# Optimization experiments

Measured on AMD Instinct MI355X. Metric: run time of the kernel, lower is better.

The kernel has to match this reference:

```python
import jax, jax.numpy as jnp
import numpy as np

FEATURE_SIZE = 512
NUM_CLASSES = 64
HIDDEN = 256
BATCH = 256
SEQ_LEN = 512


def setup_inputs() -> dict:
    key = jax.random.key(0)
    ks = jax.random.split(key, 8)
    in_dim = FEATURE_SIZE + NUM_CLASSES
    s = 0.05
    return {
        "x": jax.random.normal(ks[0], (BATCH, SEQ_LEN, FEATURE_SIZE), dtype=jnp.float32),
        "tag": jax.random.randint(ks[1], (BATCH, SEQ_LEN), 0, NUM_CLASSES, dtype=jnp.int32),
        # LSTM params, torch gate order (i, f, g, o)
        "W_ih": jax.random.normal(ks[2], (4 * HIDDEN, in_dim), dtype=jnp.float32) * s,
        "W_hh": jax.random.normal(ks[3], (4 * HIDDEN, HIDDEN), dtype=jnp.float32) * s,
        "b_ih": jax.random.normal(ks[4], (4 * HIDDEN,), dtype=jnp.float32) * s,
        "b_hh": jax.random.normal(ks[5], (4 * HIDDEN,), dtype=jnp.float32) * s,
        # output projection
        "W_out": jax.random.normal(ks[6], (NUM_CLASSES, HIDDEN), dtype=jnp.float32) * s,
        "b_out": jax.random.normal(ks[7], (NUM_CLASSES,), dtype=jnp.float32) * s,
    }


def reference(x, tag, W_ih, W_hh, b_ih, b_hh, W_out, b_out):
    # x: [B, S, F], tag: [B, S] -> scalar summed CE loss (ignore_index=-1).
    # Dropout omitted (eval-mode identity) for a deterministic reference.
    B, S, F = x.shape
    C = W_out.shape[0]
    xs = jnp.transpose(x, (1, 0, 2))      # [S, B, F] time-major
    tags = jnp.transpose(tag, (1, 0))     # [S, B]

    h0 = jnp.zeros((B, HIDDEN), dtype=x.dtype)
    c0 = jnp.zeros((B, HIDDEN), dtype=x.dtype)
    p0 = jnp.zeros((B,), dtype=jnp.int32)  # initial prev_tag = 0

    def step(carry, inputs):
        h, c, pred = carry
        xi, ti = inputs                         # [B,F], [B]
        onehot = jax.nn.one_hot(pred, C, dtype=xi.dtype)
        inp = jnp.concatenate([xi, onehot], axis=1)          # [B, F+C]
        gates = inp @ W_ih.T + b_ih + h @ W_hh.T + b_hh      # [B, 4H]
        i_g, f_g, g_g, o_g = jnp.split(gates, 4, axis=1)
        i_g = jax.nn.sigmoid(i_g)
        f_g = jax.nn.sigmoid(f_g)
        g_g = jnp.tanh(g_g)
        o_g = jax.nn.sigmoid(o_g)
        c_new = f_g * c + i_g * g_g
        h_new = o_g * jnp.tanh(c_new)
        logits = h_new @ W_out.T + b_out                     # [B, C]
        pred_new = jnp.argmax(logits, axis=1).astype(jnp.int32)
        logp = jax.nn.log_softmax(logits, axis=1)
        valid = ti != -1
        ti_safe = jnp.where(valid, ti, 0)
        nll = -jnp.take_along_axis(logp, ti_safe[:, None], axis=1)[:, 0]
        loss = jnp.sum(jnp.where(valid, nll, 0.0))
        return (h_new, c_new, pred_new), loss

    _, losses = jax.lax.scan(step, (h0, c0, p0), (xs, tags))
    return jnp.sum(losses)
```

## Files before the change

kernel.cpp:

```cpp
#include <hip/hip_runtime.h>

typedef unsigned int u32;
typedef unsigned short u16;
typedef short bf16x8 __attribute__((ext_vector_type(8)));
typedef u16 u16x8 __attribute__((ext_vector_type(8)));
typedef float f32x4 __attribute__((ext_vector_type(4)));
typedef _Float16 h2v __attribute__((ext_vector_type(2)));

#define HID 256
#define NCLS 64
#define GATES 1024
#define SEQ 512
#define NBATCH 256
#define FEAT 512
#define INDIM 576

__device__ __forceinline__ u16 f2b(float f) {
  u32 u = __builtin_bit_cast(u32, f);
  u += 0x7fffu + ((u >> 16) & 1u);
  return (u16)(u >> 16);
}
__device__ __forceinline__ float b2f(u16 v) {
  u32 u = ((u32)v) << 16;
  return __builtin_bit_cast(float, u);
}
__device__ __forceinline__ u32 packh2(float a, float b) {
  u16 lo = __builtin_bit_cast(u16, (_Float16)a);
  u16 hi = __builtin_bit_cast(u16, (_Float16)b);
  return (u32)lo | ((u32)hi << 16);
}
__device__ __forceinline__ float fdot2a(u32 h, u32 w, float c) {
#if __has_builtin(__builtin_amdgcn_fdot2)
  return __builtin_amdgcn_fdot2(__builtin_bit_cast(h2v, h),
                                __builtin_bit_cast(h2v, w), c, false);
#else
  h2v a = __builtin_bit_cast(h2v, h);
  h2v b = __builtin_bit_cast(h2v, w);
  return c + (float)a[0] * (float)b[0] + (float)a[1] * (float)b[1];
#endif
}
__device__ __forceinline__ float sigmf_(float x) { return 1.f / (1.f + __expf(-x)); }
__device__ __forceinline__ float tanhf_(float x) { return 1.f - 2.f / (1.f + __expf(2.f * x)); }

__global__ void prep_kernel(const float* __restrict__ W_ih, const float* __restrict__ W_hh,
                            const float* __restrict__ W_out,
                            u16* __restrict__ Wihk, u32* __restrict__ WhhF,
                            u32* __restrict__ WhhL2, u32* __restrict__ WoutR,
                            float* __restrict__ Woh2, float* __restrict__ out) {
  int idx = blockIdx.x * 256 + threadIdx.x;
  const int N0 = 1024 * 512;
  const int N1 = N0 + 48 * 512 * 4;
  const int N2 = N1 + 16 * 512 * 4;
  const int N3 = N2 + 16 * 512;
  const int N4 = N3 + 64 * 256 * 4;
  if (idx < N0) {
    int g = idx >> 9, k = idx & 511;
    Wihk[idx] = f2b(W_ih[g * INDIM + k]);
  } else if (idx < N1) {
    int r = idx - N0;
    int q = r & 3, u4 = r >> 2;
    int t = u4 & 511, i = u4 >> 9;
    int j = i >> 3, qq = i & 7;
    int kqv = t >> 7, glv = t & 127;
    int g = glv + j * 128;
    int k = kqv * 64 + qq * 8 + 2 * q;
    WhhF[r] = packh2(W_hh[g * HID + k], W_hh[g * HID + k + 1]);
  } else if (idx < N2) {
    int r = idx - N1;
    int q = r & 3, u4 = r >> 2;
    int t = u4 & 511, i2 = u4 >> 9;
    int j = 6 + (i2 >> 3), qq = i2 & 7;
    int kqv = t >> 7, glv = t & 127;
    int g = glv + j * 128;
    int k = kqv * 64 + qq * 8 + 2 * q;
    WhhL2[r] = packh2(W_hh[g * HID + k], W_hh[g * HID + k + 1]);
  } else if (idx < N3) {
    int r = idx - N2;
    int j = r >> 9, t = r & 511;
    int cc = t & 63, kqv = t >> 6;
    int k0 = kqv * 32 + 2 * j;
    WoutR[r] = packh2(W_out[cc * HID + k0], W_out[cc * HID + k0 + 1]);
  } else if (idx < N4) {
    int r = idx - N3;
    int jj = r & 3, c = (r >> 2) & 255, p = r >> 10;
    Woh2[r] = W_ih[(jj * 256 + c) * INDIM + FEAT + p];
  } else if (idx == N4) {
    out[0] = 0.f;
  }
}

__global__ __launch_bounds__(256) void gemm_xp(const float* __restrict__ x,
                                               const u16* __restrict__ Wihk,
                                               const float* __restrict__ b_ih,
                                               const float* __restrict__ b_hh,
                                               u16* __restrict__ Xp) {
  __shared__ u16 As[128 * 32];
  __shared__ u16 Bs[128 * 32];
  const int tid = threadIdx.x;
  const int bx = blockIdx.x;
  const int m0 = (bx >> 3) * 128;
  const int n0 = (bx & 7) * 128;
  const int wave = tid >> 6, lane = tid & 63;
  const int wm = (wave >> 1) * 64, wn = (wave & 1) * 64;
  const int l16 = lane & 15, quad = lane >> 4;
  const int r = tid >> 2;
  const int c8 = (tid & 3) * 8;

  f32x4 zero4 = {0.f, 0.f, 0.f, 0.f};
  f32x4 acc[4][4];
#pragma unroll
  for (int i = 0; i < 4; ++i)
#pragma unroll
    for (int j = 0; j < 4; ++j) acc[i][j] = zero4;

  for (int k0 = 0; k0 < FEAT; k0 += 32) {
#pragma unroll
    for (int p = 0; p < 2; ++p) {
      const float* src = x + (size_t)(m0 + r + p * 64) * FEAT + k0 + c8;
      float4 f0 = *(const float4*)src;
      float4 f1 = *(const float4*)(src + 4);
      u16x8 v;
      v[0] = f2b(f0.x); v[1] = f2b(f0.y); v[2] = f2b(f0.z); v[3] = f2b(f0.w);
      v[4] = f2b(f1.x); v[5] = f2b(f1.y); v[6] = f2b(f1.z); v[7] = f2b(f1.w);
      *(u16x8*)&As[(r + p * 64) * 32 + c8] = v;
    }
#pragma unroll
    for (int p = 0; p < 2; ++p) {
      *(uint4*)&Bs[(r + p * 64) * 32 + c8] =
          *(const uint4*)&Wihk[(size_t)(n0 + r + p * 64) * FEAT + k0 + c8];
    }
    __syncthreads();
    bf16x8 am[4], bn[4];
#pragma unroll
    for (int i = 0; i < 4; ++i)
      am[i] = *(const bf16x8*)&As[(wm + i * 16 + l16) * 32 + quad * 8];
#pragma unroll
    for (int j = 0; j < 4; ++j)
      bn[j] = *(const bf16x8*)&Bs[(wn + j * 16 + l16) * 32 + quad * 8];
#pragma unroll
    for (int i = 0; i < 4; ++i)
#pragma unroll
      for (int j = 0; j < 4; ++j)
        acc[i][j] = __builtin_amdgcn_mfma_f32_16x16x32_bf16(am[i], bn[j], acc[i][j], 0, 0, 0);
    __syncthreads();
  }

  float bias[4];
  int cols[4];
#pragma unroll
  for (int j = 0; j < 4; ++j) {
    cols[j] = n0 + wn + j * 16 + l16;
    bias[j] = b_ih[cols[j]] + b_hh[cols[j]];
  }
#pragma unroll
  for (int i = 0; i < 4; ++i) {
    int rowb = m0 + wm + i * 16 + quad * 4;
#pragma unroll
    for (int j = 0; j < 4; ++j) {
      int pcol = ((cols[j] & 255) << 2) + (cols[j] >> 8);
#pragma unroll
      for (int rr = 0; rr < 4; ++rr) {
        Xp[(size_t)(rowb + rr) * GATES + pcol] = f2b(acc[i][j][rr] + bias[j]);
      }
    }
  }
}

__global__ __launch_bounds__(512, 2) void lstm_seq(
    const u16* __restrict__ Xp, const uint4* __restrict__ WhhF,
    const uint4* __restrict__ WhhL2, const u32* __restrict__ WoutR,
    const float4* __restrict__ Woh2, const float* __restrict__ b_out,
    const int* __restrict__ tag, float* __restrict__ out) {
  extern __shared__ u32 smem[];
  uint4* whhl = (uint4*)smem;
  float* pA   = (float*)(smem + 32768);
  u32*  h_u32 = smem + 36864;
  float* pbuf = (float*)(smem + 36992);
  int*  tag_l = (int*)(smem + 37504);
  int*  predv = (int*)(smem + 38016);

  const int tid = threadIdx.x;
  const int b = blockIdx.x;
  const int kq = tid >> 7;
  const int gl = tid & 127;

  uint4 wr[48];
#pragma unroll
  for (int i = 0; i < 48; ++i) wr[i] = WhhF[i * 512 + tid];
  u32 wo[16];
#pragma unroll
  for (int i = 0; i < 16; ++i) wo[i] = WoutR[i * 512 + tid];
#pragma unroll
  for (int i = 0; i < 16; ++i) whhl[i * 512 + tid] = WhhL2[i * 512 + tid];
  tag_l[tid] = tag[b * SEQ + tid];
  if (tid < 128) h_u32[tid] = 0u;
  if (tid == 0) predv[0] = 0;
  float c_reg = 0.f;
  float bout_c = (tid < 128) ? b_out[tid & 63] : 0.f;
  float loss_acc = 0.f;
  const u16* xp_row = Xp + (size_t)b * SEQ * GATES;
  ushort4 xp_c = make_ushort4(0, 0, 0, 0);
  if (tid < 256) xp_c = *(const ushort4*)(xp_row + tid * 4);
  __syncthreads();

#pragma unroll 1
  for (int s = 0; s < SEQ; ++s) {
    int pred = predv[0];
    float4 woh4 = make_float4(0.f, 0.f, 0.f, 0.f);
    ushort4 xp_n = xp_c;
    if (tid < 256) {
      woh4 = Woh2[pred * 256 + tid];
      int sn = (s + 1 < SEQ) ? s + 1 : s;
      xp_n = *(const ushort4*)(xp_row + (size_t)sn * GATES + tid * 4);
    }

    float acc[8];
#pragma unroll
    for (int j = 0; j < 8; ++j) acc[j] = 0.f;
#pragma unroll
    for (int qq = 0; qq < 8; ++qq) {
      uint4 h4 = *(const uint4*)(h_u32 + kq * 32 + qq * 4);
      uint4 w6 = whhl[qq * 512 + tid];
      uint4 w7 = whhl[(8 + qq) * 512 + tid];
      u32 ha[4] = {h4.x, h4.y, h4.z, h4.w};
#pragma unroll
      for (int j = 0; j < 6; ++j) {
        uint4 wj = wr[j * 8 + qq];
        acc[j] = fdot2a(ha[0], wj.x, acc[j]);
        acc[j] = fdot2a(ha[1], wj.y, acc[j]);
        acc[j] = fdot2a(ha[2], wj.z, acc[j]);
        acc[j] = fdot2a(ha[3], wj.w, acc[j]);
      }
      acc[6] = fdot2a(ha[0], w6.x, acc[6]);
      acc[6] = fdot2a(ha[1], w6.y, acc[6]);
      acc[6] = fdot2a(ha[2], w6.z, acc[6]);
      acc[6] = fdot2a(ha[3], w6.w, acc[6]);
      acc[7] = fdot2a(ha[0], w7.x, acc[7]);
      acc[7] = fdot2a(ha[1], w7.y, acc[7]);
      acc[7] = fdot2a(ha[2], w7.z, acc[7]);
      acc[7] = fdot2a(ha[3], w7.w, acc[7]);
    }
#pragma unroll
    for (int j = 0; j < 8; ++j) pA[kq * 1024 + gl + j * 128] = acc[j];
    __syncthreads();

    if (tid < 256) {
      float ig = pA[tid]       + pA[1024 + tid] + pA[2048 + tid] + pA[3072 + tid]
               + b2f(xp_c.x) + woh4.x;
      float fg = pA[256 + tid] + pA[1280 + tid] + pA[2304 + tid] + pA[3328 + tid]
               + b2f(xp_c.y) + woh4.y;
      float gg = pA[512 + tid] + pA[1536 + tid] + pA[2560 + tid] + pA[3584 + tid]
               + b2f(xp_c.z) + woh4.z;
      float og = pA[768 + tid] + pA[1792 + tid] + pA[2816 + tid] + pA[3840 + tid]
               + b2f(xp_c.w) + woh4.w;
      float iv = sigmf_(ig), fv = sigmf_(fg), gv = tanhf_(gg), ov = sigmf_(og);
      c_reg = fv * c_reg + iv * gv;
      float h = ov * tanhf_(c_reg);
      ((u16*)h_u32)[tid] = __builtin_bit_cast(u16, (_Float16)h);
    }
    __syncthreads();

    {
      int kq8 = tid >> 6;
      float p = 0.f;
#pragma unroll
      for (int c = 0; c < 4; ++c) {
        uint4 h4 = *(const uint4*)(h_u32 + kq8 * 16 + c * 4);
        u32 ha2[4] = {h4.x, h4.y, h4.z, h4.w};
#pragma unroll
        for (int q = 0; q < 4; ++q) p = fdot2a(ha2[q], wo[c * 4 + q], p);
      }
      pbuf[tid] = p;
    }
    __syncthreads();

    if (tid < 128) {
      int cls = tid & 63;
      float lg = bout_c;
#pragma unroll
      for (int k = 0; k < 8; ++k) lg += pbuf[k * 64 + cls];
      if (tid < 64) {
        float v = lg; int ii = cls;
#pragma unroll
        for (int off = 32; off; off >>= 1) {
          float ov = __shfl_xor(v, off);
          int oi = __shfl_xor(ii, off);
          if (ov > v || (ov == v && oi < ii)) { v = ov; ii = oi; }
        }
        if (tid == 0) predv[0] = ii;
      } else {
        float v = lg;
#pragma unroll
        for (int off = 32; off; off >>= 1) v = fmaxf(v, __shfl_xor(v, off));
        float ssum = __expf(lg - v);
#pragma unroll
        for (int off = 32; off; off >>= 1) ssum += __shfl_xor(ssum, off);
        int t = tag_l[s];
        float lt = __shfl(lg, t & 63);
        if (t >= 0) loss_acc += v + __logf(ssum) - lt;
      }
    }
    xp_c = xp_n;
    __syncthreads();
  }
  if (tid == 64) atomicAdd(out, loss_acc);
}

extern "C" void kernel_launch(void* const* d_in, const int* in_sizes, int n_in,
                              void* d_out, int out_size, void* d_ws, size_t ws_size,
                              hipStream_t stream) {
  const float* x     = (const float*)d_in[0];
  const int*   tag   = (const int*)d_in[1];
  const float* W_ih  = (const float*)d_in[2];
  const float* W_hh  = (const float*)d_in[3];
  const float* b_ih  = (const float*)d_in[4];
  const float* b_hh  = (const float*)d_in[5];
  const float* W_out = (const float*)d_in[6];
  const float* b_out = (const float*)d_in[7];
  float* out = (float*)d_out;

  char* w = (char*)d_ws;
  u16* Xp      = (u16*)w;
  u16* Wihk    = (u16*)(w + 268435456ull);
  u32* WhhF    = (u32*)(w + 269484032ull);
  u32* WhhL2   = (u32*)(w + 269877248ull);
  u32* WoutR   = (u32*)(w + 270008320ull);
  float* Woh2  = (float*)(w + 270041088ull);

  const int smem_bytes = 38017 * 4;
  (void)hipFuncSetAttribute((const void*)lstm_seq,
                            hipFuncAttributeMaxDynamicSharedMemorySize, smem_bytes);

  prep_kernel<<<2849, 256, 0, stream>>>(W_ih, W_hh, W_out, Wihk, WhhF, WhhL2, WoutR, Woh2, out);
  gemm_xp<<<8192, 256, 0, stream>>>(x, Wihk, b_ih, b_hh, Xp);
  lstm_seq<<<256, 512, smem_bytes, stream>>>(Xp, (const uint4*)WhhF, (const uint4*)WhhL2,
                                             WoutR, (const float4*)Woh2, b_out, tag, out);
}
```

Before: 2.577 ms.

## Reduce LSTM step barriers via shuffle gate reduction and redundant argmax

Remaps the recurrent weight layout so the four K-quarter partial sums of each gate sit in adjacent lanes and are reduced with xor shuffles instead of a shared-memory partial buffer plus a barrier. Every thread now computes two hidden units' cell updates (redundantly across the 4 lanes), h is double-buffered in padded LDS, and each wave recomputes the logits reduction and argmax at the start of the next step. This cuts per-step barriers from four to two and removes the shared pred variable, at the cost of redundant transcendental and reduction work in every lane.

New measurement: 3.014 ms. 1.17x slower.

```diff
diff --git a/kernel.cpp b/kernel.cpp
--- a/kernel.cpp
+++ b/kernel.cpp
@@ -61,7 +61,7 @@
     int q = r & 3, u4 = r >> 2;
     int t = u4 & 511, i = u4 >> 9;
     int j = i >> 3, qq = i & 7;
-    int kqv = t >> 7, glv = t & 127;
+    int kqv = t & 3, glv = t >> 2;
     int g = glv + j * 128;
     int k = kqv * 64 + qq * 8 + 2 * q;
     WhhF[r] = packh2(W_hh[g * HID + k], W_hh[g * HID + k + 1]);
@@ -70,7 +70,7 @@
     int q = r & 3, u4 = r >> 2;
     int t = u4 & 511, i2 = u4 >> 9;
     int j = 6 + (i2 >> 3), qq = i2 & 7;
-    int kqv = t >> 7, glv = t & 127;
+    int kqv = t & 3, glv = t >> 2;
     int g = glv + j * 128;
     int k = kqv * 64 + qq * 8 + 2 * q;
     WhhL2[r] = packh2(W_hh[g * HID + k], W_hh[g * HID + k + 1]);
@@ -173,16 +173,16 @@
     const int* __restrict__ tag, float* __restrict__ out) {
   extern __shared__ u32 smem[];
   uint4* whhl = (uint4*)smem;
-  float* pA   = (float*)(smem + 32768);
-  u32*  h_u32 = smem + 36864;
-  float* pbuf = (float*)(smem + 36992);
-  int*  tag_l = (int*)(smem + 37504);
-  int*  predv = (int*)(smem + 38016);
+  u32*  hbase = smem + 32768;
+  float* pbuf = (float*)(smem + 33056);
+  int*  tag_l = (int*)(smem + 33568);
 
   const int tid = threadIdx.x;
   const int b = blockIdx.x;
-  const int kq = tid >> 7;
-  const int gl = tid & 127;
+  const int kq = tid & 3;
+  const int h1 = tid >> 2;
+  const int h2 = h1 + 128;
+  const int w8 = tid >> 6;
 
   uint4 wr[48];
 #pragma unroll
@@ -193,33 +193,53 @@
 #pragma unroll
   for (int i = 0; i < 16; ++i) whhl[i * 512 + tid] = WhhL2[i * 512 + tid];
   tag_l[tid] = tag[b * SEQ + tid];
-  if (tid < 128) h_u32[tid] = 0u;
-  if (tid == 0) predv[0] = 0;
-  float c_reg = 0.f;
-  float bout_c = (tid < 128) ? b_out[tid & 63] : 0.f;
+  if (tid < 288) hbase[tid] = 0u;
+  float c1 = 0.f, c2 = 0.f;
+  float bout_c = b_out[tid & 63];
   float loss_acc = 0.f;
   const u16* xp_row = Xp + (size_t)b * SEQ * GATES;
-  ushort4 xp_c = make_ushort4(0, 0, 0, 0);
-  if (tid < 256) xp_c = *(const ushort4*)(xp_row + tid * 4);
+  ushort4 xcA = *(const ushort4*)(xp_row + h1 * 4);
+  ushort4 xcB = *(const ushort4*)(xp_row + h2 * 4);
   __syncthreads();
 
 #pragma unroll 1
   for (int s = 0; s < SEQ; ++s) {
-    int pred = predv[0];
-    float4 woh4 = make_float4(0.f, 0.f, 0.f, 0.f);
-    ushort4 xp_n = xp_c;
-    if (tid < 256) {
-      woh4 = Woh2[pred * 256 + tid];
-      int sn = (s + 1 < SEQ) ? s + 1 : s;
-      xp_n = *(const ushort4*)(xp_row + (size_t)sn * GATES + tid * 4);
-    }
-
+    int pred = 0;
+    if (s > 0) {
+      int l6 = tid & 63;
+      float lg = bout_c;
+#pragma unroll
+      for (int k = 0; k < 8; ++k) lg += pbuf[k * 64 + l6];
+      float v = lg; int ii = l6;
+#pragma unroll
+      for (int off = 32; off; off >>= 1) {
+        float ov = __shfl_xor(v, off);
+        int oi = __shfl_xor(ii, off);
+        if (ov > v || (ov == v && oi < ii)) { v = ov; ii = oi; }
+      }
+      pred = ii;
+      if (w8 == 1) {
+        float ssum = __expf(lg - v);
+#pragma unroll
+        for (int off = 32; off; off >>= 1) ssum += __shfl_xor(ssum, off);
+        int t = tag_l[s - 1];
+        float lt = __shfl(lg, t & 63);
+        if (t >= 0) loss_acc += v + __logf(ssum) - lt;
+      }
+    }
+    float4 wohA = Woh2[pred * 256 + h1];
+    float4 wohB = Woh2[pred * 256 + h2];
+    int sn = (s + 1 < SEQ) ? s + 1 : s;
+    ushort4 xnA = *(const ushort4*)(xp_row + (size_t)sn * GATES + h1 * 4);
+    ushort4 xnB = *(const ushort4*)(xp_row + (size_t)sn * GATES + h2 * 4);
+
+    const u32* hbr = hbase + ((s & 1) ^ 1) * 144;
     float acc[8];
 #pragma unroll
     for (int j = 0; j < 8; ++j) acc[j] = 0.f;
 #pragma unroll
     for (int qq = 0; qq < 8; ++qq) {
-      uint4 h4 = *(const uint4*)(h_u32 + kq * 32 + qq * 4);
+      uint4 h4 = *(const uint4*)(hbr + kq * 36 + qq * 4);
       uint4 w6 = whhl[qq * 512 + tid];
       uint4 w7 = whhl[(8 + qq) * 512 + tid];
       u32 ha[4] = {h4.x, h4.y, h4.z, h4.w};
@@ -241,69 +261,75 @@
       acc[7] = fdot2a(ha[3], w7.w, acc[7]);
     }
 #pragma unroll
-    for (int j = 0; j < 8; ++j) pA[kq * 1024 + gl + j * 128] = acc[j];
+    for (int j = 0; j < 8; ++j) {
+      acc[j] += __shfl_xor(acc[j], 1);
+      acc[j] += __shfl_xor(acc[j], 2);
+    }
+    {
+      float gi = acc[0] + b2f(xcA.x) + wohA.x;
+      float gf = acc[2] + b2f(xcA.y) + wohA.y;
+      float gg = acc[4] + b2f(xcA.z) + wohA.z;
+      float go = acc[6] + b2f(xcA.w) + wohA.w;
+      float iv = sigmf_(gi), fv = sigmf_(gf), gv = tanhf_(gg), ov = sigmf_(go);
+      c1 = fv * c1 + iv * gv;
+      float hv = ov * tanhf_(c1);
+      if ((tid & 3) == 0) {
+        u16* hw = (u16*)(hbase + (s & 1) * 144);
+        int pi = h1 >> 1;
+        hw[((h1 >> 6) * 36 + (pi & 31)) * 2 + (h1 & 1)] =
+            __builtin_bit_cast(u16, (_Float16)hv);
+      }
+    }
+    {
+      float gi = acc[1] + b2f(xcB.x) + wohB.x;
+      float gf = acc[3] + b2f(xcB.y) + wohB.y;
+      float gg = acc[5] + b2f(xcB.z) + wohB.z;
+      float go = acc[7] + b2f(xcB.w) + wohB.w;
+      float iv = sigmf_(gi), fv = sigmf_(gf), gv = tanhf_(gg), ov = sigmf_(go);
+      c2 = fv * c2 + iv * gv;
+      float hv = ov * tanhf_(c2);
+      if ((tid & 3) == 0) {
+        u16* hw = (u16*)(hbase + (s & 1) * 144);
+        int pi = h2 >> 1;
+        hw[((h2 >> 6) * 36 + (pi & 31)) * 2 + (h2 & 1)] =
+            __builtin_bit_cast(u16, (_Float16)hv);
+      }
+    }
     __syncthreads();
 
-    if (tid < 256) {
-      float ig = pA[tid]       + pA[1024 + tid] + pA[2048 + tid] + pA[3072 + tid]
-               + b2f(xp_c.x) + woh4.x;
-      float fg = pA[256 + tid] + pA[1280 + tid] + pA[2304 + tid] + pA[3328 + tid]
-               + b2f(xp_c.y) + woh4.y;
-      float gg = pA[512 + tid] + pA[1536 + tid] + pA[2560 + tid] + pA[3584 + tid]
-               + b2f(xp_c.z) + woh4.z;
-      float og = pA[768 + tid] + pA[1792 + tid] + pA[2816 + tid] + pA[3840 + tid]
-               + b2f(xp_c.w) + woh4.w;
-      float iv = sigmf_(ig), fv = sigmf_(fg), gv = tanhf_(gg), ov = sigmf_(og);
-      c_reg = fv * c_reg + iv * gv;
-      float h = ov * tanhf_(c_reg);
-      ((u16*)h_u32)[tid] = __builtin_bit_cast(u16, (_Float16)h);
-    }
+    {
+      const u32* hbc = hbase + (s & 1) * 144;
+      float p = 0.f;
+#pragma unroll
+      for (int c = 0; c < 4; ++c) {
+        uint4 h4 = *(const uint4*)(hbc + (w8 >> 1) * 36 + (w8 & 1) * 16 + c * 4);
+        p = fdot2a(h4.x, wo[c * 4 + 0], p);
+        p = fdot2a(h4.y, wo[c * 4 + 1], p);
+        p = fdot2a(h4.z, wo[c * 4 + 2], p);
+        p = fdot2a(h4.w, wo[c * 4 + 3], p);
+      }
+      pbuf[tid] = p;
+    }
+    xcA = xnA; xcB = xnB;
     __syncthreads();
-
-    {
-      int kq8 = tid >> 6;
-      float p = 0.f;
-#pragma unroll
-      for (int c = 0; c < 4; ++c) {
-        uint4 h4 = *(const uint4*)(h_u32 + kq8 * 16 + c * 4);
-        u32 ha2[4] = {h4.x, h4.y, h4.z, h4.w};
-#pragma unroll
-        for (int q = 0; q < 4; ++q) p = fdot2a(ha2[q], wo[c * 4 + q], p);
-      }
-      pbuf[tid] = p;
-    }
-    __syncthreads();
-
-    if (tid < 128) {
-      int cls = tid & 63;
-      float lg = bout_c;
-#pragma unroll
-      for (int k = 0; k < 8; ++k) lg += pbuf[k * 64 + cls];
-      if (tid < 64) {
-        float v = lg; int ii = cls;
-#pragma unroll
-        for (int off = 32; off; off >>= 1) {
-          float ov = __shfl_xor(v, off);
-          int oi = __shfl_xor(ii, off);
-          if (ov > v || (ov == v && oi < ii)) { v = ov; ii = oi; }
-        }
-        if (tid == 0) predv[0] = ii;
-      } else {
-        float v = lg;
-#pragma unroll
-        for (int off = 32; off; off >>= 1) v = fmaxf(v, __shfl_xor(v, off));
-        float ssum = __expf(lg - v);
-#pragma unroll
-        for (int off = 32; off; off >>= 1) ssum += __shfl_xor(ssum, off);
-        int t = tag_l[s];
-        float lt = __shfl(lg, t & 63);
-        if (t >= 0) loss_acc += v + __logf(ssum) - lt;
-      }
-    }
-    xp_c = xp_n;
-    __syncthreads();
-  }
-  if (tid == 64) atomicAdd(out, loss_acc);
+  }
+
+  if (w8 == 1) {
+    int l6 = tid & 63;
+    float lg = bout_c;
+#pragma unroll
+    for (int k = 0; k < 8; ++k) lg += pbuf[k * 64 + l6];
+    float v = lg;
+#pragma unroll
+    for (int off = 32; off; off >>= 1) v = fmaxf(v, __shfl_xor(v, off));
+    float ssum = __expf(lg - v);
+#pragma unroll
+    for (int off = 32; off; off >>= 1) ssum += __shfl_xor(ssum, off);
+    int t = tag_l[SEQ - 1];
+    float lt = __shfl(lg, t & 63);
+    if (t >= 0) loss_acc += v + __logf(ssum) - lt;
+    if (tid == 64) atomicAdd(out, loss_acc);
+  }
 }
 
 extern "C" void kernel_launch(void* const* d_in, const int* in_sizes, int n_in,
@@ -327,7 +353,7 @@
   u32* WoutR   = (u32*)(w + 270008320ull);
   float* Woh2  = (float*)(w + 270041088ull);
 
-  const int smem_bytes = 38017 * 4;
+  const int smem_bytes = 34080 * 4;
   (void)hipFuncSetAttribute((const void*)lstm_seq,
                             hipFuncAttributeMaxDynamicSharedMemorySize, smem_bytes);
 
```

## Use 1024 threads per sequence block and keep all recurrent weights in registers

Applied to the files above, without the earlier changes.

The recurrent kernel now runs 1024 threads per batch row instead of 512, so each thread holds only 4 gate columns of W_hh (32 uint4) and 8 packed W_out words in registers. This removes the 64 KB shared-memory staging of the last two W_hh gate groups and the per-step LDS reads of those weights. The weight layouts in the prep kernel are rebuilt to match. In exchange, each step synchronises twice as many threads, the logits reduction sums 16 partials instead of 8, and the register budget per thread is tighter under the new launch bounds.

New measurement: 6.775 ms. +163.0%, slower.

```diff
diff --git a/kernel.cpp b/kernel.cpp
--- a/kernel.cpp
+++ b/kernel.cpp
@@ -45,46 +45,36 @@
 __global__ void prep_kernel(const float* __restrict__ W_ih, const float* __restrict__ W_hh,
                             const float* __restrict__ W_out,
                             u16* __restrict__ Wihk, u32* __restrict__ WhhF,
-                            u32* __restrict__ WhhL2, u32* __restrict__ WoutR,
-                            float* __restrict__ Woh2, float* __restrict__ out) {
+                            u32* __restrict__ WoutR, float* __restrict__ Woh2,
+                            float* __restrict__ out) {
   int idx = blockIdx.x * 256 + threadIdx.x;
   const int N0 = 1024 * 512;
-  const int N1 = N0 + 48 * 512 * 4;
-  const int N2 = N1 + 16 * 512 * 4;
-  const int N3 = N2 + 16 * 512;
-  const int N4 = N3 + 64 * 256 * 4;
+  const int N1 = N0 + 32 * 1024 * 4;
+  const int N2 = N1 + 8 * 1024;
+  const int N3 = N2 + 64 * 256 * 4;
   if (idx < N0) {
     int g = idx >> 9, k = idx & 511;
     Wihk[idx] = f2b(W_ih[g * INDIM + k]);
   } else if (idx < N1) {
     int r = idx - N0;
     int q = r & 3, u4 = r >> 2;
-    int t = u4 & 511, i = u4 >> 9;
+    int t = u4 & 1023, i = u4 >> 10;
     int j = i >> 3, qq = i & 7;
-    int kqv = t >> 7, glv = t & 127;
-    int g = glv + j * 128;
+    int kqv = t >> 8, glv = t & 255;
+    int g = glv + j * 256;
     int k = kqv * 64 + qq * 8 + 2 * q;
     WhhF[r] = packh2(W_hh[g * HID + k], W_hh[g * HID + k + 1]);
   } else if (idx < N2) {
     int r = idx - N1;
-    int q = r & 3, u4 = r >> 2;
-    int t = u4 & 511, i2 = u4 >> 9;
-    int j = 6 + (i2 >> 3), qq = i2 & 7;
-    int kqv = t >> 7, glv = t & 127;
-    int g = glv + j * 128;
-    int k = kqv * 64 + qq * 8 + 2 * q;
-    WhhL2[r] = packh2(W_hh[g * HID + k], W_hh[g * HID + k + 1]);
+    int i = r >> 10, t = r & 1023;
+    int cls = t & 63, kq16 = t >> 6;
+    int k0 = kq16 * 16 + 2 * i;
+    WoutR[r] = packh2(W_out[cls * HID + k0], W_out[cls * HID + k0 + 1]);
   } else if (idx < N3) {
     int r = idx - N2;
-    int j = r >> 9, t = r & 511;
-    int cc = t & 63, kqv = t >> 6;
-    int k0 = kqv * 32 + 2 * j;
-    WoutR[r] = packh2(W_out[cc * HID + k0], W_out[cc * HID + k0 + 1]);
-  } else if (idx < N4) {
-    int r = idx - N3;
     int jj = r & 3, c = (r >> 2) & 255, p = r >> 10;
     Woh2[r] = W_ih[(jj * 256 + c) * INDIM + FEAT + p];
-  } else if (idx == N4) {
+  } else if (idx == N3) {
     out[0] = 0.f;
   }
 }
@@ -166,93 +156,90 @@
   }
 }
 
-__global__ __launch_bounds__(512, 2) void lstm_seq(
+__global__ __launch_bounds__(1024, 4) void lstm_seq(
     const u16* __restrict__ Xp, const uint4* __restrict__ WhhF,
-    const uint4* __restrict__ WhhL2, const u32* __restrict__ WoutR,
-    const float4* __restrict__ Woh2, const float* __restrict__ b_out,
-    const int* __restrict__ tag, float* __restrict__ out) {
-  extern __shared__ u32 smem[];
-  uint4* whhl = (uint4*)smem;
-  float* pA   = (float*)(smem + 32768);
-  u32*  h_u32 = smem + 36864;
-  float* pbuf = (float*)(smem + 36992);
-  int*  tag_l = (int*)(smem + 37504);
-  int*  predv = (int*)(smem + 38016);
+    const u32* __restrict__ WoutR, const float4* __restrict__ Woh2,
+    const float* __restrict__ b_out, const int* __restrict__ tag,
+    float* __restrict__ out) {
+  __shared__ float pA[4096];
+  __shared__ u32 h_u32[128];
+  __shared__ float pbuf[1024];
+  __shared__ int tag_l[512];
+  __shared__ int predv;
 
   const int tid = threadIdx.x;
   const int b = blockIdx.x;
-  const int kq = tid >> 7;
-  const int gl = tid & 127;
-
-  uint4 wr[48];
-#pragma unroll
-  for (int i = 0; i < 48; ++i) wr[i] = WhhF[i * 512 + tid];
-  u32 wo[16];
-#pragma unroll
-  for (int i = 0; i < 16; ++i) wo[i] = WoutR[i * 512 + tid];
-#pragma unroll
-  for (int i = 0; i < 16; ++i) whhl[i * 512 + tid] = WhhL2[i * 512 + tid];
-  tag_l[tid] = tag[b * SEQ + tid];
+  const int kq = tid >> 8;
+  const int gl = tid & 255;
+
+  uint4 wr[32];
+#pragma unroll
+  for (int i = 0; i < 32; ++i) wr[i] = WhhF[i * 1024 + tid];
+  u32 wo[8];
+#pragma unroll
+  for (int i = 0; i < 8; ++i) wo[i] = WoutR[i * 1024 + tid];
+  if (tid < 512) tag_l[tid] = tag[b * SEQ + tid];
   if (tid < 128) h_u32[tid] = 0u;
-  if (tid == 0) predv[0] = 0;
+  if (tid == 0) predv = 0;
   float c_reg = 0.f;
-  float bout_c = (tid < 128) ? b_out[tid & 63] : 0.f;
+  float bout_c = b_out[tid & 63];
   float loss_acc = 0.f;
   const u16* xp_row = Xp + (size_t)b * SEQ * GATES;
-  ushort4 xp_c = make_ushort4(0, 0, 0, 0);
-  if (tid < 256) xp_c = *(const ushort4*)(xp_row + tid * 4);
+  ushort4 xc = make_ushort4(0, 0, 0, 0);
+  if (tid < 256) xc = *(const ushort4*)(xp_row + tid * 4);
   __syncthreads();
 
 #pragma unroll 1
   for (int s = 0; s < SEQ; ++s) {
-    int pred = predv[0];
-    float4 woh4 = make_float4(0.f, 0.f, 0.f, 0.f);
-    ushort4 xp_n = xp_c;
+    float4 woh = make_float4(0.f, 0.f, 0.f, 0.f);
+    ushort4 xn = xc;
     if (tid < 256) {
-      woh4 = Woh2[pred * 256 + tid];
+      int pred = predv;
+      woh = Woh2[pred * 256 + tid];
       int sn = (s + 1 < SEQ) ? s + 1 : s;
-      xp_n = *(const ushort4*)(xp_row + (size_t)sn * GATES + tid * 4);
-    }
-
-    float acc[8];
-#pragma unroll
-    for (int j = 0; j < 8; ++j) acc[j] = 0.f;
+      xn = *(const ushort4*)(xp_row + (size_t)sn * GATES + tid * 4);
+    }
+
+    float a0 = 0.f, a1 = 0.f, a2 = 0.f, a3 = 0.f;
 #pragma unroll
     for (int qq = 0; qq < 8; ++qq) {
       uint4 h4 = *(const uint4*)(h_u32 + kq * 32 + qq * 4);
-      uint4 w6 = whhl[qq * 512 + tid];
-      uint4 w7 = whhl[(8 + qq) * 512 + tid];
-      u32 ha[4] = {h4.x, h4.y, h4.z, h4.w};
-#pragma unroll
-      for (int j = 0; j < 6; ++j) {
-        uint4 wj = wr[j * 8 + qq];
-        acc[j] = fdot2a(ha[0], wj.x, acc[j]);
-        acc[j] = fdot2a(ha[1], wj.y, acc[j]);
-        acc[j] = fdot2a(ha[2], wj.z, acc[j]);
-        acc[j] = fdot2a(ha[3], wj.w, acc[j]);
-      }
-      acc[6] = fdot2a(ha[0], w6.x, acc[6]);
-      acc[6] = fdot2a(ha[1], w6.y, acc[6]);
-      acc[6] = fdot2a(ha[2], w6.z, acc[6]);
-      acc[6] = fdot2a(ha[3], w6.w, acc[6]);
-      acc[7] = fdot2a(ha[0], w7.x, acc[7]);
-      acc[7] = fdot2a(ha[1], w7.y, acc[7]);
-      acc[7] = fdot2a(ha[2], w7.z, acc[7]);
-      acc[7] = fdot2a(ha[3], w7.w, acc[7]);
-    }
-#pragma unroll
-    for (int j = 0; j < 8; ++j) pA[kq * 1024 + gl + j * 128] = acc[j];
+      uint4 w0 = wr[qq];
+      uint4 w1 = wr[8 + qq];
+      uint4 w2 = wr[16 + qq];
+      uint4 w3 = wr[24 + qq];
+      a0 = fdot2a(h4.x, w0.x, a0);
+      a0 = fdot2a(h4.y, w0.y, a0);
+      a0 = fdot2a(h4.z, w0.z, a0);
+      a0 = fdot2a(h4.w, w0.w, a0);
+      a1 = fdot2a(h4.x, w1.x, a1);
+      a1 = fdot2a(h4.y, w1.y, a1);
+      a1 = fdot2a(h4.z, w1.z, a1);
+      a1 = fdot2a(h4.w, w1.w, a1);
+      a2 = fdot2a(h4.x, w2.x, a2);
+      a2 = fdot2a(h4.y, w2.y, a2);
+      a2 = fdot2a(h4.z, w2.z, a2);
+      a2 = fdot2a(h4.w, w2.w, a2);
+      a3 = fdot2a(h4.x, w3.x, a3);
+      a3 = fdot2a(h4.y, w3.y, a3);
+      a3 = fdot2a(h4.z, w3.z, a3);
+      a3 = fdot2a(h4.w, w3.w, a3);
+    }
+    pA[kq * 1024 + gl]       = a0;
+    pA[kq * 1024 + 256 + gl] = a1;
+    pA[kq * 1024 + 512 + gl] = a2;
+    pA[kq * 1024 + 768 + gl] = a3;
     __syncthreads();
 
     if (tid < 256) {
       float ig = pA[tid]       + pA[1024 + tid] + pA[2048 + tid] + pA[3072 + tid]
-               + b2f(xp_c.x) + woh4.x;
+               + b2f(xc.x) + woh.x;
       float fg = pA[256 + tid] + pA[1280 + tid] + pA[2304 + tid] + pA[3328 + tid]
-               + b2f(xp_c.y) + woh4.y;
+               + b2f(xc.y) + woh.y;
       float gg = pA[512 + tid] + pA[1536 + tid] + pA[2560 + tid] + pA[3584 + tid]
-               + b2f(xp_c.z) + woh4.z;
+               + b2f(xc.z) + woh.z;
       float og = pA[768 + tid] + pA[1792 + tid] + pA[2816 + tid] + pA[3840 + tid]
-               + b2f(xp_c.w) + woh4.w;
+               + b2f(xc.w) + woh.w;
       float iv = sigmf_(ig), fv = sigmf_(fg), gv = tanhf_(gg), ov = sigmf_(og);
       c_reg = fv * c_reg + iv * gv;
       float h = ov * tanhf_(c_reg);
@@ -261,33 +248,37 @@
     __syncthreads();
 
     {
-      int kq8 = tid >> 6;
+      int kq16 = tid >> 6;
+      uint4 ha = *(const uint4*)(h_u32 + kq16 * 8);
+      uint4 hb = *(const uint4*)(h_u32 + kq16 * 8 + 4);
       float p = 0.f;
-#pragma unroll
-      for (int c = 0; c < 4; ++c) {
-        uint4 h4 = *(const uint4*)(h_u32 + kq8 * 16 + c * 4);
-        u32 ha2[4] = {h4.x, h4.y, h4.z, h4.w};
-#pragma unroll
-        for (int q = 0; q < 4; ++q) p = fdot2a(ha2[q], wo[c * 4 + q], p);
-      }
+      p = fdot2a(ha.x, wo[0], p);
+      p = fdot2a(ha.y, wo[1], p);
+      p = fdot2a(ha.z, wo[2], p);
+      p = fdot2a(ha.w, wo[3], p);
+      p = fdot2a(hb.x, wo[4], p);
+      p = fdot2a(hb.y, wo[5], p);
+      p = fdot2a(hb.z, wo[6], p);
+      p = fdot2a(hb.w, wo[7], p);
       pbuf[tid] = p;
     }
+    xc = xn;
     __syncthreads();
 
     if (tid < 128) {
-      int cls = tid & 63;
+      int l6 = tid & 63;
       float lg = bout_c;
 #pragma unroll
-      for (int k = 0; k < 8; ++k) lg += pbuf[k * 64 + cls];
+      for (int k = 0; k < 16; ++k) lg += pbuf[k * 64 + l6];
       if (tid < 64) {
-        float v = lg; int ii = cls;
+        float v = lg; int ii = l6;
 #pragma unroll
         for (int off = 32; off; off >>= 1) {
           float ov = __shfl_xor(v, off);
           int oi = __shfl_xor(ii, off);
           if (ov > v || (ov == v && oi < ii)) { v = ov; ii = oi; }
         }
-        if (tid == 0) predv[0] = ii;
+        if (tid == 0) predv = ii;
       } else {
         float v = lg;
 #pragma unroll
@@ -300,7 +291,6 @@
         if (t >= 0) loss_acc += v + __logf(ssum) - lt;
       }
     }
-    xp_c = xp_n;
     __syncthreads();
   }
   if (tid == 64) atomicAdd(out, loss_acc);
@@ -323,16 +313,11 @@
   u16* Xp      = (u16*)w;
   u16* Wihk    = (u16*)(w + 268435456ull);
   u32* WhhF    = (u32*)(w + 269484032ull);
-  u32* WhhL2   = (u32*)(w + 269877248ull);
   u32* WoutR   = (u32*)(w + 270008320ull);
   float* Woh2  = (float*)(w + 270041088ull);
 
-  const int smem_bytes = 38017 * 4;
-  (void)hipFuncSetAttribute((const void*)lstm_seq,
-                            hipFuncAttributeMaxDynamicSharedMemorySize, smem_bytes);
-
-  prep_kernel<<<2849, 256, 0, stream>>>(W_ih, W_hh, W_out, Wihk, WhhF, WhhL2, WoutR, Woh2, out);
+  prep_kernel<<<2849, 256, 0, stream>>>(W_ih, W_hh, W_out, Wihk, WhhF, WoutR, Woh2, out);
   gemm_xp<<<8192, 256, 0, stream>>>(x, Wihk, b_ih, b_hh, Xp);
-  lstm_seq<<<256, 512, smem_bytes, stream>>>(Xp, (const uint4*)WhhF, (const uint4*)WhhL2,
-                                             WoutR, (const float4*)Woh2, b_out, tag, out);
-}
+  lstm_seq<<<256, 1024, 0, stream>>>(Xp, (const uint4*)WhhF, WoutR,
+                                     (const float4*)Woh2, b_out, tag, out);
+}
```

## Defer argmax/loss to next step to drop one barrier per timestep

Applied to the files above, without the earlier changes.

Moves the logits reduction, argmax and loss computation for step s-1 to the start of step s, overlapped with the recurrent matvec. Wave 0 computes the argmax and stages the selected one-hot contribution row into shared memory, removing the separate barrier and the dependent global load per step. The h loads in the matvec are also batched in groups of four. This adds shared memory and an epilogue for the last step, and relies on the next existing barrier to order the wohv writes before they are read.

New measurement: 2.211 ms. -14.2%, faster.

```diff
diff --git a/kernel.cpp b/kernel.cpp
--- a/kernel.cpp
+++ b/kernel.cpp
@@ -177,12 +177,14 @@
   u32*  h_u32 = smem + 36864;
   float* pbuf = (float*)(smem + 36992);
   int*  tag_l = (int*)(smem + 37504);
-  int*  predv = (int*)(smem + 38016);
+  float4* wohv = (float4*)(smem + 38016);
 
   const int tid = threadIdx.x;
   const int b = blockIdx.x;
   const int kq = tid >> 7;
   const int gl = tid & 127;
+  const int wave = tid >> 6;
+  const int lane = tid & 63;
 
   uint4 wr[48];
 #pragma unroll
@@ -194,116 +196,144 @@
   for (int i = 0; i < 16; ++i) whhl[i * 512 + tid] = WhhL2[i * 512 + tid];
   tag_l[tid] = tag[b * SEQ + tid];
   if (tid < 128) h_u32[tid] = 0u;
-  if (tid == 0) predv[0] = 0;
+  if (tid < 256) wohv[tid] = Woh2[tid];
   float c_reg = 0.f;
-  float bout_c = (tid < 128) ? b_out[tid & 63] : 0.f;
+  float bout_c = b_out[tid & 63];
   float loss_acc = 0.f;
   const u16* xp_row = Xp + (size_t)b * SEQ * GATES;
-  ushort4 xp_c = make_ushort4(0, 0, 0, 0);
-  if (tid < 256) xp_c = *(const ushort4*)(xp_row + tid * 4);
+  ushort4 xc = make_ushort4(0, 0, 0, 0);
+  if (tid < 256) xc = *(const ushort4*)(xp_row + tid * 4);
   __syncthreads();
+
+  const uint4* wb0 = whhl + tid;
+  const uint4* wb1 = whhl + 4096 + tid;
 
 #pragma unroll 1
   for (int s = 0; s < SEQ; ++s) {
-    int pred = predv[0];
-    float4 woh4 = make_float4(0.f, 0.f, 0.f, 0.f);
-    ushort4 xp_n = xp_c;
+    ushort4 xn = xc;
     if (tid < 256) {
-      woh4 = Woh2[pred * 256 + tid];
       int sn = (s + 1 < SEQ) ? s + 1 : s;
-      xp_n = *(const ushort4*)(xp_row + (size_t)sn * GATES + tid * 4);
-    }
-
-    float acc[8];
-#pragma unroll
-    for (int j = 0; j < 8; ++j) acc[j] = 0.f;
-#pragma unroll
-    for (int qq = 0; qq < 8; ++qq) {
-      uint4 h4 = *(const uint4*)(h_u32 + kq * 32 + qq * 4);
-      uint4 w6 = whhl[qq * 512 + tid];
-      uint4 w7 = whhl[(8 + qq) * 512 + tid];
-      u32 ha[4] = {h4.x, h4.y, h4.z, h4.w};
-#pragma unroll
-      for (int j = 0; j < 6; ++j) {
-        uint4 wj = wr[j * 8 + qq];
-        acc[j] = fdot2a(ha[0], wj.x, acc[j]);
-        acc[j] = fdot2a(ha[1], wj.y, acc[j]);
-        acc[j] = fdot2a(ha[2], wj.z, acc[j]);
-        acc[j] = fdot2a(ha[3], wj.w, acc[j]);
-      }
-      acc[6] = fdot2a(ha[0], w6.x, acc[6]);
-      acc[6] = fdot2a(ha[1], w6.y, acc[6]);
-      acc[6] = fdot2a(ha[2], w6.z, acc[6]);
-      acc[6] = fdot2a(ha[3], w6.w, acc[6]);
-      acc[7] = fdot2a(ha[0], w7.x, acc[7]);
-      acc[7] = fdot2a(ha[1], w7.y, acc[7]);
-      acc[7] = fdot2a(ha[2], w7.z, acc[7]);
-      acc[7] = fdot2a(ha[3], w7.w, acc[7]);
-    }
-#pragma unroll
-    for (int j = 0; j < 8; ++j) pA[kq * 1024 + gl + j * 128] = acc[j];
-    __syncthreads();
-
-    if (tid < 256) {
-      float ig = pA[tid]       + pA[1024 + tid] + pA[2048 + tid] + pA[3072 + tid]
-               + b2f(xp_c.x) + woh4.x;
-      float fg = pA[256 + tid] + pA[1280 + tid] + pA[2304 + tid] + pA[3328 + tid]
-               + b2f(xp_c.y) + woh4.y;
-      float gg = pA[512 + tid] + pA[1536 + tid] + pA[2560 + tid] + pA[3584 + tid]
-               + b2f(xp_c.z) + woh4.z;
-      float og = pA[768 + tid] + pA[1792 + tid] + pA[2816 + tid] + pA[3840 + tid]
-               + b2f(xp_c.w) + woh4.w;
-      float iv = sigmf_(ig), fv = sigmf_(fg), gv = tanhf_(gg), ov = sigmf_(og);
-      c_reg = fv * c_reg + iv * gv;
-      float h = ov * tanhf_(c_reg);
-      ((u16*)h_u32)[tid] = __builtin_bit_cast(u16, (_Float16)h);
-    }
-    __syncthreads();
-
-    {
-      int kq8 = tid >> 6;
-      float p = 0.f;
-#pragma unroll
-      for (int c = 0; c < 4; ++c) {
-        uint4 h4 = *(const uint4*)(h_u32 + kq8 * 16 + c * 4);
-        u32 ha2[4] = {h4.x, h4.y, h4.z, h4.w};
-#pragma unroll
-        for (int q = 0; q < 4; ++q) p = fdot2a(ha2[q], wo[c * 4 + q], p);
-      }
-      pbuf[tid] = p;
-    }
-    __syncthreads();
-
-    if (tid < 128) {
-      int cls = tid & 63;
-      float lg = bout_c;
-#pragma unroll
-      for (int k = 0; k < 8; ++k) lg += pbuf[k * 64 + cls];
-      if (tid < 64) {
-        float v = lg; int ii = cls;
+      xn = *(const ushort4*)(xp_row + (size_t)sn * GATES + tid * 4);
+    }
+
+    if (s > 0) {
+      if (wave == 0) {
+        float lg = bout_c;
+#pragma unroll
+        for (int k = 0; k < 8; ++k) lg += pbuf[k * 64 + lane];
+        float v = lg; int ii = lane;
 #pragma unroll
         for (int off = 32; off; off >>= 1) {
           float ov = __shfl_xor(v, off);
           int oi = __shfl_xor(ii, off);
           if (ov > v || (ov == v && oi < ii)) { v = ov; ii = oi; }
         }
-        if (tid == 0) predv[0] = ii;
-      } else {
+#pragma unroll
+        for (int j = 0; j < 4; ++j) {
+          wohv[lane + j * 64] = Woh2[ii * 256 + lane + j * 64];
+        }
+      } else if (wave == 1) {
+        float lg = bout_c;
+#pragma unroll
+        for (int k = 0; k < 8; ++k) lg += pbuf[k * 64 + lane];
         float v = lg;
 #pragma unroll
         for (int off = 32; off; off >>= 1) v = fmaxf(v, __shfl_xor(v, off));
         float ssum = __expf(lg - v);
 #pragma unroll
         for (int off = 32; off; off >>= 1) ssum += __shfl_xor(ssum, off);
-        int t = tag_l[s];
+        int t = tag_l[s - 1];
         float lt = __shfl(lg, t & 63);
         if (t >= 0) loss_acc += v + __logf(ssum) - lt;
       }
     }
-    xp_c = xp_n;
-    __syncthreads();
-  }
-  if (tid == 64) atomicAdd(out, loss_acc);
+
+    float acc[8];
+#pragma unroll
+    for (int j = 0; j < 8; ++j) acc[j] = 0.f;
+#pragma unroll
+    for (int half = 0; half < 2; ++half) {
+      uint4 hh[4];
+#pragma unroll
+      for (int q = 0; q < 4; ++q)
+        hh[q] = *(const uint4*)(h_u32 + kq * 32 + (half * 4 + q) * 4);
+#pragma unroll
+      for (int q = 0; q < 4; ++q) {
+        const int qq = half * 4 + q;
+        uint4 w6 = wb0[qq * 512];
+        uint4 w7 = wb1[qq * 512];
+        u32 ha[4] = {hh[q].x, hh[q].y, hh[q].z, hh[q].w};
+#pragma unroll
+        for (int j = 0; j < 6; ++j) {
+          uint4 wj = wr[j * 8 + qq];
+          acc[j] = fdot2a(ha[0], wj.x, acc[j]);
+          acc[j] = fdot2a(ha[1], wj.y, acc[j]);
+          acc[j] = fdot2a(ha[2], wj.z, acc[j]);
+          acc[j] = fdot2a(ha[3], wj.w, acc[j]);
+        }
+        acc[6] = fdot2a(ha[0], w6.x, acc[6]);
+        acc[6] = fdot2a(ha[1], w6.y, acc[6]);
+        acc[6] = fdot2a(ha[2], w6.z, acc[6]);
+        acc[6] = fdot2a(ha[3], w6.w, acc[6]);
+        acc[7] = fdot2a(ha[0], w7.x, acc[7]);
+        acc[7] = fdot2a(ha[1], w7.y, acc[7]);
+        acc[7] = fdot2a(ha[2], w7.z, acc[7]);
+        acc[7] = fdot2a(ha[3], w7.w, acc[7]);
+      }
+    }
+#pragma unroll
+    for (int j = 0; j < 8; ++j) pA[kq * 1024 + gl + j * 128] = acc[j];
+    __syncthreads();
+
+    if (tid < 256) {
+      float4 woh = wohv[tid];
+      float ig = pA[tid]       + pA[1024 + tid] + pA[2048 + tid] + pA[3072 + tid]
+               + b2f(xc.x) + woh.x;
+      float fg = pA[256 + tid] + pA[1280 + tid] + pA[2304 + tid] + pA[3328 + tid]
+               + b2f(xc.y) + woh.y;
+      float gg = pA[512 + tid] + pA[1536 + tid] + pA[2560 + tid] + pA[3584 + tid]
+               + b2f(xc.z) + woh.z;
+      float og = pA[768 + tid] + pA[1792 + tid] + pA[2816 + tid] + pA[3840 + tid]
+               + b2f(xc.w) + woh.w;
+      float iv = sigmf_(ig), fv = sigmf_(fg), gv = tanhf_(gg), ov = sigmf_(og);
+      c_reg = fv * c_reg + iv * gv;
+      float h = ov * tanhf_(c_reg);
+      ((u16*)h_u32)[tid] = __builtin_bit_cast(u16, (_Float16)h);
+    }
+    __syncthreads();
+
+    {
+      int kq8 = tid >> 6;
+      float p = 0.f;
+#pragma unroll
+      for (int c = 0; c < 4; ++c) {
+        uint4 h4 = *(const uint4*)(h_u32 + kq8 * 16 + c * 4);
+        p = fdot2a(h4.x, wo[c * 4 + 0], p);
+        p = fdot2a(h4.y, wo[c * 4 + 1], p);
+        p = fdot2a(h4.z, wo[c * 4 + 2], p);
+        p = fdot2a(h4.w, wo[c * 4 + 3], p);
+      }
+      pbuf[tid] = p;
+    }
+    xc = xn;
+    __syncthreads();
+  }
+
+  if (wave == 1) {
+    float lg = bout_c;
+#pragma unroll
+    for (int k = 0; k < 8; ++k) lg += pbuf[k * 64 + lane];
+    float v = lg;
+#pragma unroll
+    for (int off = 32; off; off >>= 1) v = fmaxf(v, __shfl_xor(v, off));
+    float ssum = __expf(lg - v);
+#pragma unroll
+    for (int off = 32; off; off >>= 1) ssum += __shfl_xor(ssum, off);
+    int t = tag_l[SEQ - 1];
+    float lt = __shfl(lg, t & 63);
+    if (t >= 0) loss_acc += v + __logf(ssum) - lt;
+    if (tid == 64) atomicAdd(out, loss_acc);
+  }
 }
 
 extern "C" void kernel_launch(void* const* d_in, const int* in_sizes, int n_in,
@@ -327,7 +357,7 @@
   u32* WoutR   = (u32*)(w + 270008320ull);
   float* Woh2  = (float*)(w + 270041088ull);
 
-  const int smem_bytes = 38017 * 4;
+  const int smem_bytes = 39040 * 4;
   (void)hipFuncSetAttribute((const void*)lstm_seq,
                             hipFuncAttributeMaxDynamicSharedMemorySize, smem_bytes);
 
```
